# Optimization experiments

Hardware: AMD Instinct MI355X
Metric: run time of the kernel (lower is better)

The kernel has to match this reference:

```python
import jax, jax.numpy as jnp
import numpy as np

E, H, VS, VT, B, S, T = 256, 512, 32000, 32000, 64, 40, 40

def setup_inputs() -> dict:
    key = jax.random.key(0)
    ks = jax.random.split(key, 32)
    def n(k, shape, scale=0.05):
        return (jax.random.normal(k, shape, jnp.float32) * scale)
    return {
        "source_padded": jax.random.randint(ks[0], (B, S), 0, VS),
        "target_padded": jax.random.randint(ks[1], (B, T), 0, VT),
        "source_lengths": jax.random.randint(ks[2], (B,), 2, S + 1),
        "src_emb": n(ks[3], (VS, E)), "tgt_emb": n(ks[4], (VT, E)),
        "Wih_f": n(ks[5], (4 * H, E)), "Whh_f": n(ks[6], (4 * H, H)), "b_f": jnp.zeros((4 * H,), jnp.float32),
        "Wih_b": n(ks[7], (4 * H, E)), "Whh_b": n(ks[8], (4 * H, H)), "b_b": jnp.zeros((4 * H,), jnp.float32),
        "Wih_d": n(ks[9], (4 * H, H + E)), "Whh_d": n(ks[10], (4 * H, H)), "b_d": jnp.zeros((4 * H,), jnp.float32),
        "Whp": n(ks[11], (H, 2 * H)), "bhp": jnp.zeros((H,), jnp.float32),
        "Wcp": n(ks[12], (H, 2 * H)), "bcp": jnp.zeros((H,), jnp.float32),
        "Watt": n(ks[13], (H, 2 * H)), "batt": jnp.zeros((H,), jnp.float32),
        "Wcomb": n(ks[14], (H, 3 * H)), "bcomb": jnp.zeros((H,), jnp.float32),
        "Wvoc": n(ks[15], (VT, H)), "bvoc": jnp.zeros((VT,), jnp.float32),
    }

def _lstm_cell(x, h, c, Wih, Whh, b):
    g = x @ Wih.T + h @ Whh.T + b
    i, f, gg, o = jnp.split(g, 4, axis=-1)  # PyTorch gate order i,f,g,o
    c = jax.nn.sigmoid(f) * c + jax.nn.sigmoid(i) * jnp.tanh(gg)
    h = jax.nn.sigmoid(o) * jnp.tanh(c)
    return h, c

def _masked_scan(X, lengths, Wih, Whh, b):
    # X: [B,S,E]; emulates packed LSTM: state frozen and output zeroed past length
    Bn, Sn, _ = X.shape
    Hn = Whh.shape[1]
    def step(carry, inp):
        h, c = carry
        xt, t = inp
        hn, cn = _lstm_cell(xt, h, c, Wih, Whh, b)
        valid = (t < lengths)[:, None]
        h = jnp.where(valid, hn, h)
        c = jnp.where(valid, cn, c)
        return (h, c), jnp.where(valid, h, 0.0)
    init = (jnp.zeros((Bn, Hn), X.dtype), jnp.zeros((Bn, Hn), X.dtype))
    (h, c), outs = jax.lax.scan(step, init, (X.transpose(1, 0, 2), jnp.arange(Sn)))
    return outs.transpose(1, 0, 2), h, c

def _rev_in_len(X, lengths):
    # reverse each sequence within its own length, zeros elsewhere
    Sn = X.shape[1]
    idx = lengths[:, None] - 1 - jnp.arange(Sn)[None, :]
    g = jnp.take_along_axis(X, jnp.clip(idx, 0)[..., None], axis=1)
    return jnp.where((idx >= 0)[..., None], g, 0.0)

def _forward(source_padded, target_padded, source_lengths,
             src_emb, tgt_emb, Wih_f, Whh_f, b_f, Wih_b, Whh_b, b_b,
             Wih_d, Whh_d, b_d, Whp, bhp, Wcp, bcp, Watt, batt,
             Wcomb, bcomb, Wvoc, bvoc):
    X = src_emb[source_padded]                              # [B,S,E]
    out_f, hf, cf = _masked_scan(X, source_lengths, Wih_f, Whh_f, b_f)
    Xr = _rev_in_len(X, source_lengths)
    out_r, hb, cb = _masked_scan(Xr, source_lengths, Wih_b, Whh_b, b_b)
    out_b = _rev_in_len(out_r, source_lengths)
    enc_hidden = jnp.concatenate([out_f, out_b], axis=-1)   # [B,S,2H]
    dec_h = jnp.concatenate([hf, hb], axis=-1) @ Whp.T + bhp
    dec_c = jnp.concatenate([cf, cb], axis=-1) @ Wcp.T + bcp

    # generate_sent_masks: 1 at positions 1..len-1 (faithful to source), then masked_fill(-inf) where 1
    pos = jnp.arange(S)[None, :]
    enc_masks = (pos >= 1) & (pos < source_lengths[:, None])  # [B,S] bool

    enc_proj = enc_hidden @ Watt.T + batt                    # [B,S,H]
    Y = tgt_emb[target_padded]                               # [B,T,E]
    Hn = Whh_d.shape[1]
    o0 = jnp.zeros((B, Hn), jnp.float32)

    def dec_step(carry, y_t):
        h, c, o_prev = carry
        ybar = jnp.concatenate([y_t, o_prev], axis=-1)
        h, c = _lstm_cell(ybar, h, c, Wih_d, Whh_d, b_d)
        e = jnp.einsum('bsh,bh->bs', enc_proj, h)
        e = jnp.where(enc_masks, -jnp.inf, e)
        alpha = jax.nn.softmax(e, axis=-1)
        a = jnp.einsum('bs,bsd->bd', alpha, enc_hidden)      # [B,2H]
        U = jnp.concatenate([h, a], axis=-1)                 # [B,3H]
        O = jnp.tanh(U @ Wcomb.T + bcomb)                    # dropout eval-mode identity
        return (h, c, O), O

    _, outs = jax.lax.scan(dec_step, (dec_h, dec_c, o0), Y.transpose(1, 0, 2))  # [T,B,H]
    logits = outs @ Wvoc.T + bvoc                            # [T,B,VT]
    logp = jax.nn.log_softmax(logits, axis=-1)
    # CrossEntropyLoss(P.permute(1,2,0), target): mean NLL over all B*T positions
    tgt = target_padded.T[..., None]                         # [T,B,1]
    nll = -jnp.take_along_axis(logp, tgt, axis=-1).squeeze(-1)
    return nll.mean()

def reference(source_padded, target_padded, source_lengths,
              src_emb, tgt_emb, Wih_f, Whh_f, b_f, Wih_b, Whh_b, b_b,
              Wih_d, Whh_d, b_d, Whp, bhp, Wcp, bcp, Watt, batt,
              Wcomb, bcomb, Wvoc, bvoc):
    return _forward(source_padded, target_padded, source_lengths,
                    src_emb, tgt_emb, Wih_f, Whh_f, b_f, Wih_b, Whh_b, b_b,
                    Wih_d, Whh_d, b_d, Whp, bhp, Wcp, bcp, Watt, batt,
                    Wcomb, bcomb, Wvoc, bvoc)
```

## Files before the change

### kernel.cpp

```cpp
#include <hip/hip_runtime.h>
#include <math.h>

#define En 256
#define Hn 512
#define Bn 64
#define Sn 40
#define Tn 40
#define VTn 32000
#define Rn (Tn*Bn)
#define NCH 500

typedef short v8s __attribute__((ext_vector_type(8)));
typedef float v4f __attribute__((ext_vector_type(4)));
typedef _Float16 h2v __attribute__((ext_vector_type(2)));

#if defined(__has_builtin)
#  if __has_builtin(__builtin_amdgcn_fdot2)
#    define HAVE_FDOT2 1
#  endif
#endif

__device__ __forceinline__ float dot4(float4 a, float4 b){
  return a.x*b.x + a.y*b.y + a.z*b.z + a.w*b.w;
}
__device__ __forceinline__ float sigm(float x){ return 1.f/(1.f+__expf(-x)); }
__device__ __forceinline__ unsigned short f2bf(float f){
  unsigned u = __float_as_uint(f);
  unsigned r = u + 0x7FFFu + ((u>>16)&1u);
  return (unsigned short)(r>>16);
}
__device__ __forceinline__ float bf2f(unsigned short u){
  return __uint_as_float(((unsigned)u)<<16);
}
__device__ __forceinline__ unsigned pkbf(float a, float b){
  return (unsigned)f2bf(a) | ((unsigned)f2bf(b)<<16);
}
__device__ __forceinline__ unsigned pkh(float a, float b){
  _Float16 ha = (_Float16)a, hb = (_Float16)b;
  unsigned short ua = __builtin_bit_cast(unsigned short, ha);
  unsigned short ub = __builtin_bit_cast(unsigned short, hb);
  return (unsigned)ua | ((unsigned)ub<<16);
}
__device__ __forceinline__ float fd2(unsigned w, unsigned h, float c){
#ifdef HAVE_FDOT2
  return __builtin_amdgcn_fdot2(__builtin_bit_cast(h2v,w), __builtin_bit_cast(h2v,h), c, false);
#else
  h2v a = __builtin_bit_cast(h2v,w), b = __builtin_bit_cast(h2v,h);
  return c + (float)a[0]*(float)b[0] + (float)a[1]*(float)b[1];
#endif
}

__global__ void prep(float* zero_base,
                     const int* __restrict__ src, const int* __restrict__ tgt,
                     const int* __restrict__ lens, int* __restrict__ grev,
                     int* __restrict__ gtgt,
                     const float* __restrict__ Whh_f, unsigned short* __restrict__ Whf16,
                     const float* __restrict__ Whh_b, unsigned short* __restrict__ Whb16,
                     const float* __restrict__ Whh_d, const float* __restrict__ Wih_d,
                     unsigned short* __restrict__ Wd16,
                     const float* __restrict__ Wcomb, unsigned short* __restrict__ Wc16){
  int blk = blockIdx.x, tid = threadIdx.x;
  if (blk < 224){
    ((float4*)zero_base)[blk*256 + tid] = make_float4(0.f,0.f,0.f,0.f);
    return;
  }
  blk -= 224;
  if (blk < 10){
    int r = blk*256 + tid;
    if (r < Bn*Sn){
      int b = r/Sn, s = r%Sn;
      int j = lens[b]-1-s;
      grev[r] = (j>=0) ? src[b*Sn+j] : -1;
      int t2 = r>>6, b2 = r&63;
      gtgt[r] = tgt[b2*Tn + t2];
    }
    return;
  }
  blk -= 10;
  if (blk < 512){
    size_t e = ((size_t)blk*256 + tid)*8;
    float4 a = *(const float4*)(Whh_f+e), b = *(const float4*)(Whh_f+e+4);
    uint4 u; u.x=pkbf(a.x,a.y); u.y=pkbf(a.z,a.w); u.z=pkbf(b.x,b.y); u.w=pkbf(b.z,b.w);
    *(uint4*)(Whf16+e) = u;
    return;
  }
  blk -= 512;
  if (blk < 512){
    size_t e = ((size_t)blk*256 + tid)*8;
    float4 a = *(const float4*)(Whh_b+e), b = *(const float4*)(Whh_b+e+4);
    uint4 u; u.x=pkbf(a.x,a.y); u.y=pkbf(a.z,a.w); u.z=pkbf(b.x,b.y); u.w=pkbf(b.z,b.w);
    *(uint4*)(Whb16+e) = u;
    return;
  }
  blk -= 512;
  if (blk < 1024){
    size_t e = ((size_t)blk*256 + tid)*8;
    int row = (int)(e>>10), k = (int)(e&1023);
    const float* sp = (k<512) ? (Whh_d + (size_t)row*512 + k)
                              : (Wih_d + (size_t)row*768 + 256 + (k-512));
    float4 a = *(const float4*)sp, b = *(const float4*)(sp+4);
    uint4 u; u.x=pkbf(a.x,a.y); u.y=pkbf(a.z,a.w); u.z=pkbf(b.x,b.y); u.w=pkbf(b.z,b.w);
    *(uint4*)(Wd16+e) = u;
    return;
  }
  blk -= 1024;
  {
    size_t e = ((size_t)blk*256 + tid)*8;
    float4 a = *(const float4*)(Wcomb+e), b = *(const float4*)(Wcomb+e+4);
    uint4 u; u.x=pkh(a.x,a.y); u.y=pkh(a.z,a.w); u.z=pkh(b.x,b.y); u.w=pkh(b.z,b.w);
    *(uint4*)(Wc16+e) = u;
  }
}

struct GArg {
  const float* A; const int* gth; int lda;
  const float* B; int ldb;
  const float* bias; float* C; int ldc; int K;
};
struct GArg3 { GArg a[3]; };

__global__ __launch_bounds__(256) void ggemm(GArg3 p3){
  GArg d = p3.a[blockIdx.z];
  __shared__ unsigned short Abf[128*64];
  __shared__ unsigned short Bbf[128*64];
  const int n0 = blockIdx.x*128, r0 = blockIdx.y*128;
  const int tid = threadIdx.x;
  const int w = tid>>6, lane = tid&63;
  const int wr = w>>1, wc = w&1;
  v4f acc[4][4];
#pragma unroll
  for (int i=0;i<4;++i)
#pragma unroll
    for (int j=0;j<4;++j) acc[i][j] = (v4f){0.f,0.f,0.f,0.f};
  const int srow = tid>>1, kc = (tid&1)*32;
  int ar = d.gth ? d.gth[r0+srow] : (r0+srow);
  const float* Arow = (ar>=0) ? (d.A + (size_t)ar*d.lda) : nullptr;
  const float* Brow = d.B + (size_t)(n0+srow)*d.ldb;
  for (int kb=0; kb<d.K; kb+=64){
    __syncthreads();
#pragma unroll
    for (int c=0;c<4;++c){
      int k = kc + c*8;
      int swz = k ^ ((srow&7)<<3);
      uint4 ua;
      if (Arow){
        float4 x0 = *(const float4*)(Arow+kb+k);
        float4 x1 = *(const float4*)(Arow+kb+k+4);
        ua.x=pkbf(x0.x,x0.y); ua.y=pkbf(x0.z,x0.w); ua.z=pkbf(x1.x,x1.y); ua.w=pkbf(x1.z,x1.w);
      } else ua = make_uint4(0,0,0,0);
      *(uint4*)&Abf[srow*64 + swz] = ua;
      float4 y0 = *(const float4*)(Brow+kb+k);
      float4 y1 = *(const float4*)(Brow+kb+k+4);
      uint4 ub; ub.x=pkbf(y0.x,y0.y); ub.y=pkbf(y0.z,y0.w); ub.z=pkbf(y1.x,y1.y); ub.w=pkbf(y1.z,y1.w);
      *(uint4*)&Bbf[srow*64 + swz] = ub;
    }
    __syncthreads();
#pragma unroll
    for (int kk=0; kk<64; kk+=32){
      int kfr = kk + (lane>>4)*8;
      v8s bfr[4];
#pragma unroll
      for (int ni=0;ni<4;++ni){
        int brow = wc*64 + ni*16 + (lane&15);
        bfr[ni] = *(const v8s*)&Bbf[brow*64 + (kfr ^ ((brow&7)<<3))];
      }
#pragma unroll
      for (int mi=0;mi<4;++mi){
        int arl = wr*64 + mi*16 + (lane&15);
        v8s af = *(const v8s*)&Abf[arl*64 + (kfr ^ ((arl&7)<<3))];
#pragma unroll
        for (int ni=0;ni<4;++ni)
          acc[mi][ni] = __builtin_amdgcn_mfma_f32_16x16x32_bf16(af, bfr[ni], acc[mi][ni], 0,0,0);
      }
    }
  }
#pragma unroll
  for (int ni=0;ni<4;++ni){
    int col = n0 + wc*64 + ni*16 + (lane&15);
    float bb = d.bias[col];
#pragma unroll
    for (int mi=0;mi<4;++mi)
#pragma unroll
      for (int r=0;r<4;++r){
        int row = r0 + wr*64 + mi*16 + (lane>>4)*4 + r;
        d.C[(size_t)row*d.ldc + col] = acc[mi][ni][r] + bb;
      }
  }
}

__global__ __launch_bounds__(256) void enc_step(
    const unsigned short* __restrict__ hf_in, unsigned short* __restrict__ hf_out,
    const unsigned short* __restrict__ hb_in, unsigned short* __restrict__ hb_out,
    float* __restrict__ cF, float* __restrict__ cB,
    const unsigned short* __restrict__ Wf16, const unsigned short* __restrict__ Wb16,
    const float* __restrict__ Gf, const float* __restrict__ Gb,
    float* __restrict__ encH, float* __restrict__ outR,
    const int* __restrict__ lens, int s){
  __shared__ unsigned short Wls[64*64];
  __shared__ unsigned short Hls[64*64];
  __shared__ float Cls[64][66];
  const int bx = blockIdx.x;
  const int dir = bx>>5;
  const int u0 = (bx&31)*16;
  const unsigned short* W16 = dir ? Wb16 : Wf16;
  const unsigned short* hin = dir ? hb_in : hf_in;
  unsigned short* hout      = dir ? hb_out : hf_out;
  float* c = dir ? cB : cF;
  const float* G = dir ? Gb : Gf;
  const int tid = threadIdx.x, w = tid>>6, lane = tid&63;
  v4f acc[4];
#pragma unroll
  for (int ni=0;ni<4;++ni) acc[ni] = (v4f){0.f,0.f,0.f,0.f};
  const int l = tid>>2;
  const int kc4 = (tid&3)*16;
  const int grow = (l>>4)*512 + u0 + (l&15);
  const unsigned short* Wrow = W16 + (size_t)grow*512;
  const unsigned short* Hrow = hin + (size_t)l*512;
  for (int kb=0; kb<512; kb+=64){
    __syncthreads();
#pragma unroll
    for (int c2=0;c2<2;++c2){
      int k = kc4 + c2*8;
      int swz = k ^ ((l&7)<<3);
      *(uint4*)&Wls[l*64+swz] = *(const uint4*)(Wrow + kb + k);
      *(uint4*)&Hls[l*64+swz] = *(const uint4*)(Hrow + kb + k);
    }
    __syncthreads();
#pragma unroll
    for (int kk=0; kk<64; kk+=32){
      int kfr = kk + (lane>>4)*8;
      int mrow = w*16 + (lane&15);
      v8s af = *(const v8s*)&Wls[mrow*64 + (kfr ^ ((mrow&7)<<3))];
#pragma unroll
      for (int ni=0;ni<4;++ni){
        int brow = ni*16 + (lane&15);
        v8s bf = *(const v8s*)&Hls[brow*64 + (kfr ^ ((brow&7)<<3))];
        acc[ni] = __builtin_amdgcn_mfma_f32_16x16x32_bf16(af, bf, acc[ni], 0,0,0);
      }
    }
  }
#pragma unroll
  for (int ni=0;ni<4;++ni)
#pragma unroll
    for (int r=0;r<4;++r)
      Cls[w*16 + (lane>>4)*4 + r][ni*16 + (lane&15)] = acc[ni][r];
  __syncthreads();
  const int u_l = tid&15, bq = tid>>4;
#pragma unroll
  for (int j=0;j<4;++j){
    int b = bq + j*16;
    size_t gidx = ((size_t)(b*Sn+s))*2048 + u0 + u_l;
    float gi = Cls[u_l][b]      + G[gidx];
    float gf = Cls[16+u_l][b]   + G[gidx+512];
    float gg = Cls[32+u_l][b]   + G[gidx+1024];
    float go = Cls[48+u_l][b]   + G[gidx+1536];
    int bu = b*512 + u0 + u_l;
    bool valid = s < lens[b];
    float cp = c[bu];
    float cn = sigm(gf)*cp + sigm(gi)*tanhf(gg);
    float hn = sigm(go)*tanhf(cn);
    c[bu] = valid ? cn : cp;
    hout[bu] = valid ? f2bf(hn) : hin[bu];
    if (dir==0) encH[((size_t)(b*Sn+s))*1024 + u0+u_l] = valid ? hn : 0.f;
    else        outR[((size_t)(b*Sn+s))*512  + u0+u_l] = valid ? hn : 0.f;
  }
}

__global__ void mid_fused(const unsigned short* __restrict__ h16f,
                          const unsigned short* __restrict__ h16b,
                          const float* __restrict__ cF, const float* __restrict__ cB,
                          const float* __restrict__ Whp, const float* __restrict__ bhp,
                          const float* __restrict__ Wcp, const float* __restrict__ bcp,
                          unsigned short* __restrict__ ho0, float* __restrict__ dC,
                          const float* __restrict__ outR, const int* __restrict__ lens,
                          float* __restrict__ encH,
                          const float* __restrict__ Wvoc, unsigned short* __restrict__ W16){
  int blk = blockIdx.x, tid = threadIdx.x;
  if (blk < 128){
    int isC = blk >= 64;
    int idx = (blk & 63)*256 + tid;
#pragma unroll
    for (int e=0;e<2;++e){
      int o = idx*2 + e;
      int b = o>>9, u = o&511;
      if (!isC){
        const float* wr = Whp + (size_t)u*1024;
        float acc = bhp[u];
        const uint4* hf4 = (const uint4*)(h16f + (size_t)b*512);
        for (int q=0;q<64;++q){
          uint4 v = hf4[q];
          unsigned uu[4] = {v.x,v.y,v.z,v.w};
#pragma unroll
          for (int i2=0;i2<4;++i2){
            acc += bf2f((unsigned short)(uu[i2]&0xFFFF))*wr[q*8+i2*2];
            acc += bf2f((unsigned short)(uu[i2]>>16))   *wr[q*8+i2*2+1];
          }
        }
        const uint4* hb4 = (const uint4*)(h16b + (size_t)b*512);
        const float* wr2 = wr + 512;
        for (int q=0;q<64;++q){
          uint4 v = hb4[q];
          unsigned uu[4] = {v.x,v.y,v.z,v.w};
#pragma unroll
          for (int i2=0;i2<4;++i2){
            acc += bf2f((unsigned short)(uu[i2]&0xFFFF))*wr2[q*8+i2*2];
            acc += bf2f((unsigned short)(uu[i2]>>16))   *wr2[q*8+i2*2+1];
          }
        }
        ho0[b*1024 + u] = f2bf(acc);
      } else {
        const float4* w4 = (const float4*)(Wcp + (size_t)u*1024);
        float acc = bcp[u];
        const float4* x1 = (const float4*)(cF + (size_t)b*512);
        const float4* x2 = (const float4*)(cB + (size_t)b*512);
        for (int q=0;q<128;++q) acc += dot4(x1[q], w4[q]);
        for (int q=0;q<128;++q) acc += dot4(x2[q], w4[128+q]);
        dC[b*512 + u] = acc;
      }
    }
    return;
  }
  blk -= 128;
  if (blk < 640){
    int e = (blk*256 + tid)*8;
    int u = e & 511;
    int bsi = e >> 9;
    int s = bsi % Sn, b = bsi / Sn;
    int len = lens[b];
    float4 v0 = make_float4(0,0,0,0), v1 = make_float4(0,0,0,0);
    if (s < len){
      int j = len-1-s;
      const float* sp = outR + ((size_t)(b*Sn+j))*512 + u;
      v0 = *(const float4*)sp; v1 = *(const float4*)(sp+4);
    }
    float* dp = encH + ((size_t)(b*Sn+s))*1024 + 512 + u;
    *(float4*)dp = v0; *(float4*)(dp+4) = v1;
    return;
  }
  blk -= 640;
  {
    size_t e = ((size_t)blk*256 + tid)*8;
    float4 a = *(const float4*)(Wvoc+e), b = *(const float4*)(Wvoc+e+4);
    uint4 u; u.x=pkbf(a.x,a.y); u.y=pkbf(a.z,a.w); u.z=pkbf(b.x,b.y); u.w=pkbf(b.z,b.w);
    *(uint4*)(W16+e) = u;
  }
}

__global__ __launch_bounds__(256) void dec_gates(
    const unsigned short* __restrict__ Wd16, const unsigned short* __restrict__ ho_cur,
    unsigned short* __restrict__ ho_next, const float* __restrict__ Gdy,
    float* __restrict__ dC, int t){
  __shared__ unsigned short Wls[64*64];
  __shared__ unsigned short Hls[64*64];
  __shared__ float Cls[64][66];
  const int u0 = blockIdx.x*16;
  const int tid = threadIdx.x, w = tid>>6, lane = tid&63;
  v4f acc[4];
#pragma unroll
  for (int ni=0;ni<4;++ni) acc[ni] = (v4f){0.f,0.f,0.f,0.f};
  const int l = tid>>2;
  const int kc4 = (tid&3)*16;
  const int grow = (l>>4)*512 + u0 + (l&15);
  const unsigned short* Wrow = Wd16 + (size_t)grow*1024;
  const unsigned short* Hrow = ho_cur + (size_t)l*1024;
  for (int kb=0; kb<1024; kb+=64){
    __syncthreads();
#pragma unroll
    for (int c2=0;c2<2;++c2){
      int k = kc4 + c2*8;
      int swz = k ^ ((l&7)<<3);
      *(uint4*)&Wls[l*64+swz] = *(const uint4*)(Wrow + kb + k);
      *(uint4*)&Hls[l*64+swz] = *(const uint4*)(Hrow + kb + k);
    }
    __syncthreads();
#pragma unroll
    for (int kk=0; kk<64; kk+=32){
      int kfr = kk + (lane>>4)*8;
      int mrow = w*16 + (lane&15);
      v8s af = *(const v8s*)&Wls[mrow*64 + (kfr ^ ((mrow&7)<<3))];
#pragma unroll
      for (int ni=0;ni<4;++ni){
        int brow = ni*16 + (lane&15);
        v8s bf = *(const v8s*)&Hls[brow*64 + (kfr ^ ((brow&7)<<3))];
        acc[ni] = __builtin_amdgcn_mfma_f32_16x16x32_bf16(af, bf, acc[ni], 0,0,0);
      }
    }
  }
#pragma unroll
  for (int ni=0;ni<4;++ni)
#pragma unroll
    for (int r=0;r<4;++r)
      Cls[w*16 + (lane>>4)*4 + r][ni*16 + (lane&15)] = acc[ni][r];
  __syncthreads();
  const int u_l = tid&15, bq = tid>>4;
#pragma unroll
  for (int j=0;j<4;++j){
    int b = bq + j*16;
    size_t gidx = ((size_t)(t*Bn+b))*2048 + u0 + u_l;
    float gi = Cls[u_l][b]      + Gdy[gidx];
    float gf = Cls[16+u_l][b]   + Gdy[gidx+512];
    float gg = Cls[32+u_l][b]   + Gdy[gidx+1024];
    float go = Cls[48+u_l][b]   + Gdy[gidx+1536];
    int bu = b*512 + u0 + u_l;
    float cp = dC[bu];
    float cn = sigm(gf)*cp + sigm(gi)*tanhf(gg);
    float hn = sigm(go)*tanhf(cn);
    dC[bu] = cn;
    ho_next[b*1024 + u0 + u_l] = f2bf(hn);
  }
}

__global__ __launch_bounds__(256) void dec_attcomb(
    unsigned short* __restrict__ ho_next, const float* __restrict__ eprj,
    const float* __restrict__ encH, const int* __restrict__ lens,
    const unsigned short* __restrict__ Wc16, const float* __restrict__ bcomb,
    unsigned short* __restrict__ A16, int t){
  const int b = blockIdx.x >> 2;
  const int q = blockIdx.x & 3;
  const int tid = threadIdx.x;
  __shared__ __align__(16) float hs[512];
  __shared__ __align__(16) float als[1024];
  __shared__ float es[Sn], sal[Sn];
  __shared__ float sinv;
  __shared__ __align__(16) unsigned int ha16[768];
  __shared__ float ps[128][2];
  for (int i=tid; i<512; i+=256) hs[i] = bf2f(ho_next[b*1024 + i]);
  __syncthreads();
  const int wv = tid>>6, lane = tid&63;
  const int len = lens[b];
  for (int si=0; si<10; ++si){
    int s2 = wv*10 + si;
    const float* pr = eprj + ((size_t)(b*Sn+s2))*512 + lane*8;
    float4 p0 = *(const float4*)pr, p1 = *(const float4*)(pr+4);
    const float* hh = hs + lane*8;
    float4 h0 = *(const float4*)hh, h1 = *(const float4*)(hh+4);
    float a = dot4(p0,h0) + dot4(p1,h1);
#pragma unroll
    for (int off=32; off; off>>=1) a += __shfl_down(a, off);
    if (lane==0) es[s2] = (s2>=1 && s2<len) ? -INFINITY : a;
  }
  __syncthreads();
  if (tid < 64){
    float e2 = (tid<Sn) ? es[tid] : -INFINITY;
    float m = e2;
#pragma unroll
    for (int off=32; off; off>>=1) m = fmaxf(m, __shfl_xor(m, off));
    float p = (tid<Sn) ? __expf(e2-m) : 0.f;
    float sum = p;
#pragma unroll
    for (int off=32; off; off>>=1) sum += __shfl_xor(sum, off);
    if (tid<Sn) sal[tid] = p;
    if (tid==0) sinv = 1.f/sum;
  }
  __syncthreads();
  float inv = sinv;
#pragma unroll
  for (int dq=0; dq<4; ++dq){
    int d = dq*256 + tid;
    float acc = 0.f;
    for (int s2=0; s2<Sn; ++s2) acc += sal[s2]*encH[((size_t)(b*Sn+s2))*1024 + d];
    als[d] = acc*inv;
  }
  __syncthreads();
  for (int p=tid; p<768; p+=256){
    int i0 = 2*p, i1 = 2*p+1;
    float x0 = (i0<512) ? hs[i0] : als[i0-512];
    float x1 = (i1<512) ? hs[i1] : als[i1-512];
    ha16[p] = pkh(x0, x1);
  }
  __syncthreads();
  const int rloc = tid & 127;
  const int kh = tid >> 7;
  const int row = q*128 + rloc;
  const uint4* wp = (const uint4*)(Wc16 + (size_t)row*1536 + kh*768);
  const uint4* hp = (const uint4*)&ha16[kh*384];
  float a0 = 0.f;
#pragma unroll 4
  for (int qq=0; qq<96; ++qq){
    uint4 wv4 = wp[qq];
    uint4 hv4 = hp[qq];
    a0 = fd2(wv4.x, hv4.x, a0);
    a0 = fd2(wv4.y, hv4.y, a0);
    a0 = fd2(wv4.z, hv4.z, a0);
    a0 = fd2(wv4.w, hv4.w, a0);
  }
  ps[rloc][kh] = a0;
  __syncthreads();
  if (tid < 128){
    int r2 = q*128 + tid;
    float O = tanhf(ps[tid][0] + ps[tid][1] + bcomb[r2]);
    unsigned short ob = f2bf(O);
    ho_next[b*1024 + 512 + r2] = ob;
    A16[((size_t)(t*Bn+b))*512 + r2] = ob;
  }
}

__global__ __launch_bounds__(256,1) void vocab_mfma(
    const unsigned short* __restrict__ A16, const unsigned short* __restrict__ W16,
    const float* __restrict__ bv, float* __restrict__ stats){
  __shared__ unsigned short Abf[256*64];
  __shared__ unsigned short Bbf[128*64];
  const int vb = blockIdx.x, rb = blockIdx.y;
  const int r0 = rb*256, v0 = vb*128;
  const int tid = threadIdx.x, w = tid>>6, lane = tid&63;
  const int wr = w>>1, wc = w&1;
  v4f acc[8][4];
#pragma unroll
  for (int i=0;i<8;++i)
#pragma unroll
    for (int j=0;j<4;++j) acc[i][j] = (v4f){0.f,0.f,0.f,0.f};
  const unsigned short* Arow = A16 + (size_t)(r0+tid)*512;
  const int srow2 = tid>>1, kc2 = (tid&1)*32;
  const unsigned short* Brow = W16 + (size_t)(v0+srow2)*512;
  for (int kb=0; kb<512; kb+=64){
    __syncthreads();
#pragma unroll
    for (int c=0;c<8;++c){
      int k = c*8;
      *(uint4*)&Abf[tid*64 + (k ^ ((tid&7)<<3))] = *(const uint4*)(Arow + kb + k);
    }
#pragma unroll
    for (int c=0;c<4;++c){
      int k = kc2 + c*8;
      *(uint4*)&Bbf[srow2*64 + (k ^ ((srow2&7)<<3))] = *(const uint4*)(Brow + kb + k);
    }
    __syncthreads();
#pragma unroll
    for (int kk=0; kk<64; kk+=32){
      int kfr = kk + (lane>>4)*8;
      v8s bfr[4];
#pragma unroll
      for (int ni=0;ni<4;++ni){
        int brow = wc*64 + ni*16 + (lane&15);
        bfr[ni] = *(const v8s*)&Bbf[brow*64 + (kfr ^ ((brow&7)<<3))];
      }
#pragma unroll
      for (int mi=0;mi<8;++mi){
        int arow = wr*128 + mi*16 + (lane&15);
        v8s af = *(const v8s*)&Abf[arow*64 + (kfr ^ ((arow&7)<<3))];
#pragma unroll
        for (int ni=0;ni<4;++ni)
          acc[mi][ni] = __builtin_amdgcn_mfma_f32_16x16x32_bf16(af, bfr[ni], acc[mi][ni], 0,0,0);
      }
    }
  }
  float bj[4];
#pragma unroll
  for (int ni=0;ni<4;++ni) bj[ni] = bv[v0 + wc*64 + ni*16 + (lane&15)];
#pragma unroll
  for (int mi=0;mi<8;++mi){
#pragma unroll
    for (int r=0;r<4;++r){
      float x0 = acc[mi][0][r]+bj[0], x1 = acc[mi][1][r]+bj[1];
      float x2 = acc[mi][2][r]+bj[2], x3 = acc[mi][3][r]+bj[3];
      float mx = fmaxf(fmaxf(x0,x1), fmaxf(x2,x3));
#pragma unroll
      for (int off=1; off<16; off<<=1) mx = fmaxf(mx, __shfl_xor(mx, off));
      float se = __expf(x0-mx)+__expf(x1-mx)+__expf(x2-mx)+__expf(x3-mx);
#pragma unroll
      for (int off=1; off<16; off<<=1) se += __shfl_xor(se, off);
      if ((lane&15)==0){
        int row = r0 + wr*128 + mi*16 + (lane>>4)*4 + r;
        int chunk = vb*2 + wc;
        size_t o = ((size_t)row*NCH + chunk)*2;
        stats[o] = mx; stats[o+1] = se;
      }
    }
  }
}

__global__ void tail(const float* __restrict__ stats, const unsigned short* __restrict__ A16,
                     const float* __restrict__ Wvoc, const float* __restrict__ bvoc,
                     const int* __restrict__ gtgt, float* __restrict__ out){
  int r = blockIdx.x*4 + (threadIdx.x>>6);
  int lane = threadIdx.x & 63;
  const float* st = stats + (size_t)r*NCH*2;
  float M = -INFINITY;
  for (int c=lane; c<NCH; c+=64) M = fmaxf(M, st[2*c]);
#pragma unroll
  for (int off=32; off; off>>=1) M = fmaxf(M, __shfl_xor(M, off));
  float S = 0.f;
  for (int c=lane; c<NCH; c+=64) S += __expf(st[2*c]-M)*st[2*c+1];
#pragma unroll
  for (int off=32; off; off>>=1) S += __shfl_xor(S, off);
  int v = gtgt[r];
  int k = lane*8;
  uint4 a4 = *(const uint4*)(A16 + (size_t)r*512 + k);
  const float* wvp = Wvoc + (size_t)v*512 + k;
  float4 w0 = *(const float4*)wvp, w1 = *(const float4*)(wvp+4);
  unsigned uu[4] = {a4.x, a4.y, a4.z, a4.w};
  float dot = 0.f;
  dot += bf2f((unsigned short)(uu[0]&0xFFFF))*w0.x + bf2f((unsigned short)(uu[0]>>16))*w0.y;
  dot += bf2f((unsigned short)(uu[1]&0xFFFF))*w0.z + bf2f((unsigned short)(uu[1]>>16))*w0.w;
  dot += bf2f((unsigned short)(uu[2]&0xFFFF))*w1.x + bf2f((unsigned short)(uu[2]>>16))*w1.y;
  dot += bf2f((unsigned short)(uu[3]&0xFFFF))*w1.z + bf2f((unsigned short)(uu[3]>>16))*w1.w;
#pragma unroll
  for (int off=32; off; off>>=1) dot += __shfl_down(dot, off);
  if (lane==0){
    float lse = M + logf(S);
    float nll = lse - (dot + bvoc[v]);
    atomicAdd(out, nll * (1.0f/(float)Rn));
  }
}

extern "C" void kernel_launch(void* const* d_in, const int* in_sizes, int n_in,
                              void* d_out, int out_size, void* d_ws, size_t ws_size,
                              hipStream_t stream){
  (void)in_sizes; (void)n_in; (void)out_size; (void)ws_size;
  const int*   srcP  = (const int*)  d_in[0];
  const int*   tgtP  = (const int*)  d_in[1];
  const int*   lens  = (const int*)  d_in[2];
  const float* semb  = (const float*)d_in[3];
  const float* temb  = (const float*)d_in[4];
  const float* Wih_f = (const float*)d_in[5];
  const float* Whh_f = (const float*)d_in[6];
  const float* b_f   = (const float*)d_in[7];
  const float* Wih_b = (const float*)d_in[8];
  const float* Whh_b = (const float*)d_in[9];
  const float* b_b   = (const float*)d_in[10];
  const float* Wih_d = (const float*)d_in[11];
  const float* Whh_d = (const float*)d_in[12];
  const float* b_d   = (const float*)d_in[13];
  const float* Whp   = (const float*)d_in[14];
  const float* bhp   = (const float*)d_in[15];
  const float* Wcp   = (const float*)d_in[16];
  const float* bcp   = (const float*)d_in[17];
  const float* Watt  = (const float*)d_in[18];
  const float* batt  = (const float*)d_in[19];
  const float* Wcomb = (const float*)d_in[20];
  const float* bcomb = (const float*)d_in[21];
  const float* Wvoc  = (const float*)d_in[22];
  const float* bvoc  = (const float*)d_in[23];

  float* w = (float*)d_ws;
  size_t off = 0;
  auto alloc = [&](size_t n){ float* p = w + off; off += n; return p; };
  float* encH = alloc(2621440);
  float* outR = alloc(1310720);
  float* eprj = alloc(1310720);
  float* Gf   = alloc(5242880);
  float* Gb   = alloc(5242880);
  float* Gdy  = alloc(5242880);
  unsigned short* A16   = (unsigned short*)alloc(655360);
  unsigned short* Whf16 = (unsigned short*)alloc(524288);
  unsigned short* Whb16 = (unsigned short*)alloc(524288);
  unsigned short* Wd16  = (unsigned short*)alloc(1048576);
  unsigned short* Wc16  = (unsigned short*)alloc(393216);
  float* zero_base = w + off;
  float* cF = alloc(32768);
  float* cB = alloc(32768);
  float* dC = alloc(32768);
  unsigned short* h16f[2] = {(unsigned short*)alloc(16384), (unsigned short*)alloc(16384)};
  unsigned short* h16b[2] = {(unsigned short*)alloc(16384), (unsigned short*)alloc(16384)};
  unsigned short* ho[2]   = {(unsigned short*)alloc(32768), (unsigned short*)alloc(32768)};
  int* grev = (int*)alloc(2560);
  int* gtgt = (int*)alloc(2560);
  unsigned short* W16 = (unsigned short*)Gf;
  float* stats = encH;

  hipMemsetAsync(d_out, 0, sizeof(float), stream);
  prep<<<2666, 256, 0, stream>>>(zero_base, srcP, tgtP, lens, grev, gtgt,
                                 Whh_f, Whf16, Whh_b, Whb16, Whh_d, Wih_d, Wd16,
                                 Wcomb, Wc16);
  {
    GArg3 g;
    g.a[0] = GArg{semb, srcP, En, Wih_f, En,  b_f, Gf,  2048, En};
    g.a[1] = GArg{semb, grev, En, Wih_b, En,  b_b, Gb,  2048, En};
    g.a[2] = GArg{temb, gtgt, En, Wih_d, 768, b_d, Gdy, 2048, En};
    ggemm<<<dim3(16,20,3), 256, 0, stream>>>(g);
  }
  for (int s=0; s<Sn; ++s)
    enc_step<<<64, 256, 0, stream>>>(h16f[s&1], h16f[(s+1)&1], h16b[s&1], h16b[(s+1)&1],
                                     cF, cB, Whf16, Whb16, Gf, Gb, encH, outR, lens, s);
  mid_fused<<<8768, 256, 0, stream>>>(h16f[0], h16b[0], cF, cB, Whp, bhp, Wcp, bcp,
                                      ho[0], dC, outR, lens, encH, Wvoc, W16);
  {
    GArg3 g;
    g.a[0] = GArg{encH, nullptr, 1024, Watt, 1024, batt, eprj, 512, 1024};
    g.a[1] = g.a[0]; g.a[2] = g.a[0];
    ggemm<<<dim3(4,20,1), 256, 0, stream>>>(g);
  }
  for (int t=0; t<Tn; ++t){
    dec_gates<<<32, 256, 0, stream>>>(Wd16, ho[t&1], ho[(t+1)&1], Gdy, dC, t);
    dec_attcomb<<<256, 256, 0, stream>>>(ho[(t+1)&1], eprj, encH, lens, Wc16, bcomb, A16, t);
  }
  vocab_mfma<<<dim3(VTn/128, Rn/256), 256, 0, stream>>>(A16, W16, bvoc, stats);
  tail<<<Rn/4, 256, 0, stream>>>(stats, A16, Wvoc, bvoc, gtgt, (float*)d_out);
}
```

Baseline: 2.440 ms.

## Persist encoder scan with grid barrier, merge decoder steps, retile vocab GEMM

Replaces the 40 per-step encoder launches with one persistent 64-block kernel that synchronises steps through an atomic spin barrier. The decoder's gates and attention/combine kernels become one launch per step: 64 blocks compute attention output for step t-1 and 32 blocks compute gates for step t, which spin on a counter before reading the new output. The vocab GEMM drops from 256-row to 128-row tiles with a different staging layout. The intent is to cut launch overhead and overlap decoder phases; the risks are deadlock if blocks are not co-resident, spin cost, and fewer MFMA per loaded tile.

```diff
diff --git a/kernel.cpp b/kernel.cpp
--- a/kernel.cpp
+++ b/kernel.cpp
@@ -60,11 +60,11 @@
                      unsigned short* __restrict__ Wd16,
                      const float* __restrict__ Wcomb, unsigned short* __restrict__ Wc16){
   int blk = blockIdx.x, tid = threadIdx.x;
-  if (blk < 224){
+  if (blk < 209){
     ((float4*)zero_base)[blk*256 + tid] = make_float4(0.f,0.f,0.f,0.f);
     return;
   }
-  blk -= 224;
+  blk -= 209;
   if (blk < 10){
     int r = blk*256 + tid;
     if (r < Bn*Sn){
@@ -188,14 +188,14 @@
   }
 }
 
-__global__ __launch_bounds__(256) void enc_step(
-    const unsigned short* __restrict__ hf_in, unsigned short* __restrict__ hf_out,
-    const unsigned short* __restrict__ hb_in, unsigned short* __restrict__ hb_out,
+__global__ __launch_bounds__(256) void enc_scan(
+    unsigned short* __restrict__ hf0, unsigned short* __restrict__ hf1,
+    unsigned short* __restrict__ hb0, unsigned short* __restrict__ hb1,
     float* __restrict__ cF, float* __restrict__ cB,
     const unsigned short* __restrict__ Wf16, const unsigned short* __restrict__ Wb16,
     const float* __restrict__ Gf, const float* __restrict__ Gb,
     float* __restrict__ encH, float* __restrict__ outR,
-    const int* __restrict__ lens, int s){
+    const int* __restrict__ lens, int* __restrict__ bar){
   __shared__ unsigned short Wls[64*64];
   __shared__ unsigned short Hls[64*64];
   __shared__ float Cls[64][66];
@@ -203,66 +203,82 @@
   const int dir = bx>>5;
   const int u0 = (bx&31)*16;
   const unsigned short* W16 = dir ? Wb16 : Wf16;
-  const unsigned short* hin = dir ? hb_in : hf_in;
-  unsigned short* hout      = dir ? hb_out : hf_out;
   float* c = dir ? cB : cF;
   const float* G = dir ? Gb : Gf;
   const int tid = threadIdx.x, w = tid>>6, lane = tid&63;
-  v4f acc[4];
-#pragma unroll
-  for (int ni=0;ni<4;++ni) acc[ni] = (v4f){0.f,0.f,0.f,0.f};
   const int l = tid>>2;
   const int kc4 = (tid&3)*16;
   const int grow = (l>>4)*512 + u0 + (l&15);
   const unsigned short* Wrow = W16 + (size_t)grow*512;
-  const unsigned short* Hrow = hin + (size_t)l*512;
-  for (int kb=0; kb<512; kb+=64){
-    __syncthreads();
-#pragma unroll
-    for (int c2=0;c2<2;++c2){
-      int k = kc4 + c2*8;
-      int swz = k ^ ((l&7)<<3);
-      *(uint4*)&Wls[l*64+swz] = *(const uint4*)(Wrow + kb + k);
-      *(uint4*)&Hls[l*64+swz] = *(const uint4*)(Hrow + kb + k);
-    }
-    __syncthreads();
-#pragma unroll
-    for (int kk=0; kk<64; kk+=32){
-      int kfr = kk + (lane>>4)*8;
-      int mrow = w*16 + (lane&15);
-      v8s af = *(const v8s*)&Wls[mrow*64 + (kfr ^ ((mrow&7)<<3))];
-#pragma unroll
-      for (int ni=0;ni<4;++ni){
-        int brow = ni*16 + (lane&15);
-        v8s bf = *(const v8s*)&Hls[brow*64 + (kfr ^ ((brow&7)<<3))];
-        acc[ni] = __builtin_amdgcn_mfma_f32_16x16x32_bf16(af, bf, acc[ni], 0,0,0);
-      }
-    }
-  }
-#pragma unroll
-  for (int ni=0;ni<4;++ni)
-#pragma unroll
-    for (int r=0;r<4;++r)
-      Cls[w*16 + (lane>>4)*4 + r][ni*16 + (lane&15)] = acc[ni][r];
-  __syncthreads();
-  const int u_l = tid&15, bq = tid>>4;
-#pragma unroll
-  for (int j=0;j<4;++j){
-    int b = bq + j*16;
-    size_t gidx = ((size_t)(b*Sn+s))*2048 + u0 + u_l;
-    float gi = Cls[u_l][b]      + G[gidx];
-    float gf = Cls[16+u_l][b]   + G[gidx+512];
-    float gg = Cls[32+u_l][b]   + G[gidx+1024];
-    float go = Cls[48+u_l][b]   + G[gidx+1536];
-    int bu = b*512 + u0 + u_l;
-    bool valid = s < lens[b];
-    float cp = c[bu];
-    float cn = sigm(gf)*cp + sigm(gi)*tanhf(gg);
-    float hn = sigm(go)*tanhf(cn);
-    c[bu] = valid ? cn : cp;
-    hout[bu] = valid ? f2bf(hn) : hin[bu];
-    if (dir==0) encH[((size_t)(b*Sn+s))*1024 + u0+u_l] = valid ? hn : 0.f;
-    else        outR[((size_t)(b*Sn+s))*512  + u0+u_l] = valid ? hn : 0.f;
+#pragma unroll 1
+  for (int s=0; s<Sn; ++s){
+    const unsigned short* hin = dir ? ((s&1)?hb1:hb0) : ((s&1)?hf1:hf0);
+    unsigned short* hout      = dir ? ((s&1)?hb0:hb1) : ((s&1)?hf0:hf1);
+    const unsigned short* Hrow = hin + (size_t)l*512;
+    v4f acc[4];
+#pragma unroll
+    for (int ni=0;ni<4;++ni) acc[ni] = (v4f){0.f,0.f,0.f,0.f};
+    for (int kb=0; kb<512; kb+=64){
+      __syncthreads();
+#pragma unroll
+      for (int c2=0;c2<2;++c2){
+        int k = kc4 + c2*8;
+        int swz = k ^ ((l&7)<<3);
+        *(uint4*)&Wls[l*64+swz] = *(const uint4*)(Wrow + kb + k);
+        *(uint4*)&Hls[l*64+swz] = *(const uint4*)(Hrow + kb + k);
+      }
+      __syncthreads();
+#pragma unroll
+      for (int kk=0; kk<64; kk+=32){
+        int kfr = kk + (lane>>4)*8;
+        int mrow = w*16 + (lane&15);
+        v8s af = *(const v8s*)&Wls[mrow*64 + (kfr ^ ((mrow&7)<<3))];
+#pragma unroll
+        for (int ni=0;ni<4;++ni){
+          int brow = ni*16 + (lane&15);
+          v8s bf = *(const v8s*)&Hls[brow*64 + (kfr ^ ((brow&7)<<3))];
+          acc[ni] = __builtin_amdgcn_mfma_f32_16x16x32_bf16(af, bf, acc[ni], 0,0,0);
+        }
+      }
+    }
+#pragma unroll
+    for (int ni=0;ni<4;++ni)
+#pragma unroll
+      for (int r=0;r<4;++r)
+        Cls[w*16 + (lane>>4)*4 + r][ni*16 + (lane&15)] = acc[ni][r];
+    __syncthreads();
+    const int u_l = tid&15, bq = tid>>4;
+#pragma unroll
+    for (int j=0;j<4;++j){
+      int b = bq + j*16;
+      size_t gidx = ((size_t)(b*Sn+s))*2048 + u0 + u_l;
+      float gi = Cls[u_l][b]      + G[gidx];
+      float gf = Cls[16+u_l][b]   + G[gidx+512];
+      float gg = Cls[32+u_l][b]   + G[gidx+1024];
+      float go = Cls[48+u_l][b]   + G[gidx+1536];
+      int bu = b*512 + u0 + u_l;
+      bool valid = s < lens[b];
+      float cp = c[bu];
+      float cn = sigm(gf)*cp + sigm(gi)*tanhf(gg);
+      float hn = sigm(go)*tanhf(cn);
+      c[bu] = valid ? cn : cp;
+      hout[bu] = valid ? f2bf(hn) : hin[bu];
+      if (dir==0) encH[((size_t)(b*Sn+s))*1024 + u0+u_l] = valid ? hn : 0.f;
+      else        outR[((size_t)(b*Sn+s))*512  + u0+u_l] = valid ? hn : 0.f;
+    }
+    if (s < Sn-1){
+      __syncthreads();
+      if (tid==0){
+        __threadfence();
+        __hip_atomic_fetch_add(bar, 1, __ATOMIC_RELEASE, __HIP_MEMORY_SCOPE_AGENT);
+        const int target = 64*(s+1);
+        long it = 0;
+        while (__hip_atomic_load(bar, __ATOMIC_ACQUIRE, __HIP_MEMORY_SCOPE_AGENT) < target
+               && it < 2000000000L) ++it;
+      }
+      __syncthreads();
+      __threadfence();
+    }
   }
 }
 
@@ -271,7 +287,7 @@
                           const float* __restrict__ cF, const float* __restrict__ cB,
                           const float* __restrict__ Whp, const float* __restrict__ bhp,
                           const float* __restrict__ Wcp, const float* __restrict__ bcp,
-                          unsigned short* __restrict__ ho0, float* __restrict__ dC,
+                          unsigned short* __restrict__ H0, float* __restrict__ dC,
                           const float* __restrict__ outR, const int* __restrict__ lens,
                           float* __restrict__ encH,
                           const float* __restrict__ Wvoc, unsigned short* __restrict__ W16){
@@ -307,7 +323,7 @@
             acc += bf2f((unsigned short)(uu[i2]>>16))   *wr2[q*8+i2*2+1];
           }
         }
-        ho0[b*1024 + u] = f2bf(acc);
+        H0[b*512 + u] = f2bf(acc);
       } else {
         const float4* w4 = (const float4*)(Wcp + (size_t)u*1024);
         float acc = bcp[u];
@@ -346,15 +362,101 @@
   }
 }
 
-__global__ __launch_bounds__(256) void dec_gates(
-    const unsigned short* __restrict__ Wd16, const unsigned short* __restrict__ ho_cur,
-    unsigned short* __restrict__ ho_next, const float* __restrict__ Gdy,
-    float* __restrict__ dC, int t){
+__global__ __launch_bounds__(256) void dec_step(
+    const unsigned short* __restrict__ Wd16,
+    const unsigned short* __restrict__ Hcur, unsigned short* __restrict__ Hnext,
+    unsigned short* __restrict__ obuf,
+    const float* __restrict__ Gdy, float* __restrict__ dC,
+    const float* __restrict__ eprj, const float* __restrict__ encH,
+    const int* __restrict__ lens,
+    const unsigned short* __restrict__ Wc16, const float* __restrict__ bcomb,
+    unsigned short* __restrict__ A16, int* __restrict__ cnt, int t){
+  const int blk = blockIdx.x, tid = threadIdx.x;
+  if (blk < Bn){
+    if (t == 0) return;
+    const int b = blk;
+    __shared__ __align__(16) float hs[512];
+    __shared__ __align__(16) float als[1024];
+    __shared__ float es[Sn], sal[Sn];
+    __shared__ float sinv;
+    __shared__ __align__(16) unsigned ha16[768];
+    for (int i=tid; i<512; i+=256) hs[i] = bf2f(Hcur[b*512 + i]);
+    __syncthreads();
+    const int wv = tid>>6, lane = tid&63;
+    const int len = lens[b];
+    for (int si=0; si<10; ++si){
+      int s2 = wv*10 + si;
+      const float* pr = eprj + ((size_t)(b*Sn+s2))*512 + lane*8;
+      float4 p0 = *(const float4*)pr, p1 = *(const float4*)(pr+4);
+      const float* hh = hs + lane*8;
+      float4 h0 = *(const float4*)hh, h1 = *(const float4*)(hh+4);
+      float a = dot4(p0,h0) + dot4(p1,h1);
+#pragma unroll
+      for (int off=32; off; off>>=1) a += __shfl_down(a, off);
+      if (lane==0) es[s2] = (s2>=1 && s2<len) ? -INFINITY : a;
+    }
+    __syncthreads();
+    if (tid < 64){
+      float e2 = (tid<Sn) ? es[tid] : -INFINITY;
+      float m = e2;
+#pragma unroll
+      for (int off=32; off; off>>=1) m = fmaxf(m, __shfl_xor(m, off));
+      float p = (tid<Sn) ? __expf(e2-m) : 0.f;
+      float sum = p;
+#pragma unroll
+      for (int off=32; off; off>>=1) sum += __shfl_xor(sum, off);
+      if (tid<Sn) sal[tid] = p;
+      if (tid==0) sinv = 1.f/sum;
+    }
+    __syncthreads();
+    float inv = sinv;
+#pragma unroll
+    for (int dq=0; dq<4; ++dq){
+      int d = dq*256 + tid;
+      float acc = 0.f;
+      for (int s2=0; s2<Sn; ++s2) acc += sal[s2]*encH[((size_t)(b*Sn+s2))*1024 + d];
+      als[d] = acc*inv;
+    }
+    __syncthreads();
+    for (int p=tid; p<768; p+=256){
+      int i0 = 2*p, i1 = 2*p+1;
+      float x0 = (i0<512) ? hs[i0] : als[i0-512];
+      float x1 = (i1<512) ? hs[i1] : als[i1-512];
+      ha16[p] = pkh(x0, x1);
+    }
+    __syncthreads();
+    const uint4* hp = (const uint4*)ha16;
+#pragma unroll
+    for (int rr=0; rr<2; ++rr){
+      int row = tid + rr*256;
+      const uint4* wp = (const uint4*)(Wc16 + (size_t)row*1536);
+      float a0 = 0.f;
+#pragma unroll 4
+      for (int qq=0; qq<192; ++qq){
+        uint4 w4 = wp[qq];
+        uint4 h4 = hp[qq];
+        a0 = fd2(w4.x, h4.x, a0);
+        a0 = fd2(w4.y, h4.y, a0);
+        a0 = fd2(w4.z, h4.z, a0);
+        a0 = fd2(w4.w, h4.w, a0);
+      }
+      float O = tanhf(a0 + bcomb[row]);
+      unsigned short ob = f2bf(O);
+      obuf[b*512 + row] = ob;
+      A16[((size_t)((t-1)*Bn + b))*512 + row] = ob;
+    }
+    __threadfence();
+    __syncthreads();
+    if (tid==0)
+      __hip_atomic_fetch_add(&cnt[t], 1, __ATOMIC_RELEASE, __HIP_MEMORY_SCOPE_AGENT);
+    return;
+  }
+  if (t == Tn) return;
   __shared__ unsigned short Wls[64*64];
   __shared__ unsigned short Hls[64*64];
   __shared__ float Cls[64][66];
-  const int u0 = blockIdx.x*16;
-  const int tid = threadIdx.x, w = tid>>6, lane = tid&63;
+  const int u0 = (blk - Bn)*16;
+  const int w = tid>>6, lane = tid&63;
   v4f acc[4];
 #pragma unroll
   for (int ni=0;ni<4;++ni) acc[ni] = (v4f){0.f,0.f,0.f,0.f};
@@ -362,15 +464,27 @@
   const int kc4 = (tid&3)*16;
   const int grow = (l>>4)*512 + u0 + (l&15);
   const unsigned short* Wrow = Wd16 + (size_t)grow*1024;
-  const unsigned short* Hrow = ho_cur + (size_t)l*1024;
-  for (int kb=0; kb<1024; kb+=64){
+  const int kmax = t ? 1024 : 512;
+  for (int kb=0; kb<kmax; kb+=64){
+    if (kb == 512){
+      __syncthreads();
+      if (tid==0){
+        long it = 0;
+        while (__hip_atomic_load(&cnt[t], __ATOMIC_ACQUIRE, __HIP_MEMORY_SCOPE_AGENT) < Bn
+               && it < 2000000000L) ++it;
+      }
+      __syncthreads();
+      __threadfence();
+    }
+    const unsigned short* src = (kb < 512) ? (Hcur + (size_t)l*512 + kb)
+                                           : (obuf + (size_t)l*512 + (kb-512));
     __syncthreads();
 #pragma unroll
     for (int c2=0;c2<2;++c2){
       int k = kc4 + c2*8;
       int swz = k ^ ((l&7)<<3);
       *(uint4*)&Wls[l*64+swz] = *(const uint4*)(Wrow + kb + k);
-      *(uint4*)&Hls[l*64+swz] = *(const uint4*)(Hrow + kb + k);
+      *(uint4*)&Hls[l*64+swz] = *(const uint4*)(src + k);
     }
     __syncthreads();
 #pragma unroll
@@ -406,149 +520,68 @@
     float cn = sigm(gf)*cp + sigm(gi)*tanhf(gg);
     float hn = sigm(go)*tanhf(cn);
     dC[bu] = cn;
-    ho_next[b*1024 + u0 + u_l] = f2bf(hn);
-  }
-}
-
-__global__ __launch_bounds__(256) void dec_attcomb(
-    unsigned short* __restrict__ ho_next, const float* __restrict__ eprj,
-    const float* __restrict__ encH, const int* __restrict__ lens,
-    const unsigned short* __restrict__ Wc16, const float* __restrict__ bcomb,
-    unsigned short* __restrict__ A16, int t){
-  const int b = blockIdx.x >> 2;
-  const int q = blockIdx.x & 3;
-  const int tid = threadIdx.x;
-  __shared__ __align__(16) float hs[512];
-  __shared__ __align__(16) float als[1024];
-  __shared__ float es[Sn], sal[Sn];
-  __shared__ float sinv;
-  __shared__ __align__(16) unsigned int ha16[768];
-  __shared__ float ps[128][2];
-  for (int i=tid; i<512; i+=256) hs[i] = bf2f(ho_next[b*1024 + i]);
-  __syncthreads();
-  const int wv = tid>>6, lane = tid&63;
-  const int len = lens[b];
-  for (int si=0; si<10; ++si){
-    int s2 = wv*10 + si;
-    const float* pr = eprj + ((size_t)(b*Sn+s2))*512 + lane*8;
-    float4 p0 = *(const float4*)pr, p1 = *(const float4*)(pr+4);
-    const float* hh = hs + lane*8;
-    float4 h0 = *(const float4*)hh, h1 = *(const float4*)(hh+4);
-    float a = dot4(p0,h0) + dot4(p1,h1);
-#pragma unroll
-    for (int off=32; off; off>>=1) a += __shfl_down(a, off);
-    if (lane==0) es[s2] = (s2>=1 && s2<len) ? -INFINITY : a;
-  }
-  __syncthreads();
-  if (tid < 64){
-    float e2 = (tid<Sn) ? es[tid] : -INFINITY;
-    float m = e2;
-#pragma unroll
-    for (int off=32; off; off>>=1) m = fmaxf(m, __shfl_xor(m, off));
-    float p = (tid<Sn) ? __expf(e2-m) : 0.f;
-    float sum = p;
-#pragma unroll
-    for (int off=32; off; off>>=1) sum += __shfl_xor(sum, off);
-    if (tid<Sn) sal[tid] = p;
-    if (tid==0) sinv = 1.f/sum;
-  }
-  __syncthreads();
-  float inv = sinv;
-#pragma unroll
-  for (int dq=0; dq<4; ++dq){
-    int d = dq*256 + tid;
-    float acc = 0.f;
-    for (int s2=0; s2<Sn; ++s2) acc += sal[s2]*encH[((size_t)(b*Sn+s2))*1024 + d];
-    als[d] = acc*inv;
-  }
-  __syncthreads();
-  for (int p=tid; p<768; p+=256){
-    int i0 = 2*p, i1 = 2*p+1;
-    float x0 = (i0<512) ? hs[i0] : als[i0-512];
-    float x1 = (i1<512) ? hs[i1] : als[i1-512];
-    ha16[p] = pkh(x0, x1);
-  }
-  __syncthreads();
-  const int rloc = tid & 127;
-  const int kh = tid >> 7;
-  const int row = q*128 + rloc;
-  const uint4* wp = (const uint4*)(Wc16 + (size_t)row*1536 + kh*768);
-  const uint4* hp = (const uint4*)&ha16[kh*384];
-  float a0 = 0.f;
-#pragma unroll 4
-  for (int qq=0; qq<96; ++qq){
-    uint4 wv4 = wp[qq];
-    uint4 hv4 = hp[qq];
-    a0 = fd2(wv4.x, hv4.x, a0);
-    a0 = fd2(wv4.y, hv4.y, a0);
-    a0 = fd2(wv4.z, hv4.z, a0);
-    a0 = fd2(wv4.w, hv4.w, a0);
-  }
-  ps[rloc][kh] = a0;
-  __syncthreads();
-  if (tid < 128){
-    int r2 = q*128 + tid;
-    float O = tanhf(ps[tid][0] + ps[tid][1] + bcomb[r2]);
-    unsigned short ob = f2bf(O);
-    ho_next[b*1024 + 512 + r2] = ob;
-    A16[((size_t)(t*Bn+b))*512 + r2] = ob;
-  }
-}
-
-__global__ __launch_bounds__(256,1) void vocab_mfma(
+    Hnext[b*512 + u0 + u_l] = f2bf(hn);
+  }
+}
+
+__global__ __launch_bounds__(256) void vocab_mfma(
     const unsigned short* __restrict__ A16, const unsigned short* __restrict__ W16,
     const float* __restrict__ bv, float* __restrict__ stats){
-  __shared__ unsigned short Abf[256*64];
+  __shared__ unsigned short Abf[128*64];
   __shared__ unsigned short Bbf[128*64];
   const int vb = blockIdx.x, rb = blockIdx.y;
-  const int r0 = rb*256, v0 = vb*128;
-  const int tid = threadIdx.x, w = tid>>6, lane = tid&63;
+  const int r0 = rb*128, v0 = vb*128;
+  const int tid = threadIdx.x;
+  const int w = tid>>6, lane = tid&63;
   const int wr = w>>1, wc = w&1;
-  v4f acc[8][4];
-#pragma unroll
-  for (int i=0;i<8;++i)
+  v4f acc[4][4];
+#pragma unroll
+  for (int i=0;i<4;++i)
 #pragma unroll
     for (int j=0;j<4;++j) acc[i][j] = (v4f){0.f,0.f,0.f,0.f};
-  const unsigned short* Arow = A16 + (size_t)(r0+tid)*512;
-  const int srow2 = tid>>1, kc2 = (tid&1)*32;
-  const unsigned short* Brow = W16 + (size_t)(v0+srow2)*512;
-  for (int kb=0; kb<512; kb+=64){
-    __syncthreads();
-#pragma unroll
-    for (int c=0;c<8;++c){
-      int k = c*8;
-      *(uint4*)&Abf[tid*64 + (k ^ ((tid&7)<<3))] = *(const uint4*)(Arow + kb + k);
-    }
+  const int srow = tid>>1;
+  const int sk0  = (tid&1)*8;
+  const int arow = wr*64 + (lane&15);
+  const int brow = wc*64 + (lane&15);
+  const int kfrag = (lane>>4)*8;
+  for (int ks=0; ks<8; ++ks){
+    const int kb = ks*64;
+    __syncthreads();
 #pragma unroll
     for (int c=0;c<4;++c){
-      int k = kc2 + c*8;
-      *(uint4*)&Bbf[srow2*64 + (k ^ ((srow2&7)<<3))] = *(const uint4*)(Brow + kb + k);
+      int k = sk0 + c*16;
+      int swz = k ^ ((srow&7)<<3);
+      *(uint4*)&Abf[srow*64 + swz] = *(const uint4*)(A16 + (size_t)(r0+srow)*512 + kb + k);
+      *(uint4*)&Bbf[srow*64 + swz] = *(const uint4*)(W16 + (size_t)(v0+srow)*512 + kb + k);
     }
     __syncthreads();
 #pragma unroll
     for (int kk=0; kk<64; kk+=32){
-      int kfr = kk + (lane>>4)*8;
-      v8s bfr[4];
+      v8s af[4], bf[4];
+#pragma unroll
+      for (int mi=0;mi<4;++mi){
+        int row = arow + mi*16;
+        int k = kk + kfrag;
+        af[mi] = *(const v8s*)&Abf[row*64 + (k ^ ((row&7)<<3))];
+      }
 #pragma unroll
       for (int ni=0;ni<4;++ni){
-        int brow = wc*64 + ni*16 + (lane&15);
-        bfr[ni] = *(const v8s*)&Bbf[brow*64 + (kfr ^ ((brow&7)<<3))];
-      }
-#pragma unroll
-      for (int mi=0;mi<8;++mi){
-        int arow = wr*128 + mi*16 + (lane&15);
-        v8s af = *(const v8s*)&Abf[arow*64 + (kfr ^ ((arow&7)<<3))];
+        int row = brow + ni*16;
+        int k = kk + kfrag;
+        bf[ni] = *(const v8s*)&Bbf[row*64 + (k ^ ((row&7)<<3))];
+      }
+#pragma unroll
+      for (int mi=0;mi<4;++mi)
 #pragma unroll
         for (int ni=0;ni<4;++ni)
-          acc[mi][ni] = __builtin_amdgcn_mfma_f32_16x16x32_bf16(af, bfr[ni], acc[mi][ni], 0,0,0);
-      }
+          acc[mi][ni] = __builtin_amdgcn_mfma_f32_16x16x32_bf16(af[mi], bf[ni], acc[mi][ni], 0,0,0);
     }
   }
   float bj[4];
 #pragma unroll
   for (int ni=0;ni<4;++ni) bj[ni] = bv[v0 + wc*64 + ni*16 + (lane&15)];
 #pragma unroll
-  for (int mi=0;mi<8;++mi){
+  for (int mi=0;mi<4;++mi){
 #pragma unroll
     for (int r=0;r<4;++r){
       float x0 = acc[mi][0][r]+bj[0], x1 = acc[mi][1][r]+bj[1];
@@ -560,10 +593,11 @@
 #pragma unroll
       for (int off=1; off<16; off<<=1) se += __shfl_xor(se, off);
       if ((lane&15)==0){
-        int row = r0 + wr*128 + mi*16 + (lane>>4)*4 + r;
+        int row = r0 + wr*64 + mi*16 + (lane>>4)*4 + r;
         int chunk = vb*2 + wc;
         size_t o = ((size_t)row*NCH + chunk)*2;
-        stats[o] = mx; stats[o+1] = se;
+        stats[o]   = mx;
+        stats[o+1] = se;
       }
     }
   }
@@ -650,16 +684,21 @@
   float* cF = alloc(32768);
   float* cB = alloc(32768);
   float* dC = alloc(32768);
-  unsigned short* h16f[2] = {(unsigned short*)alloc(16384), (unsigned short*)alloc(16384)};
-  unsigned short* h16b[2] = {(unsigned short*)alloc(16384), (unsigned short*)alloc(16384)};
-  unsigned short* ho[2]   = {(unsigned short*)alloc(32768), (unsigned short*)alloc(32768)};
+  unsigned short* h16f0 = (unsigned short*)alloc(16384);
+  unsigned short* h16f1 = (unsigned short*)alloc(16384);
+  unsigned short* h16b0 = (unsigned short*)alloc(16384);
+  unsigned short* h16b1 = (unsigned short*)alloc(16384);
+  unsigned short* H0    = (unsigned short*)alloc(16384);
+  unsigned short* H1    = (unsigned short*)alloc(16384);
+  unsigned short* obuf  = (unsigned short*)alloc(16384);
+  int* syncv = (int*)alloc(1024);
   int* grev = (int*)alloc(2560);
   int* gtgt = (int*)alloc(2560);
   unsigned short* W16 = (unsigned short*)Gf;
   float* stats = encH;
 
   hipMemsetAsync(d_out, 0, sizeof(float), stream);
-  prep<<<2666, 256, 0, stream>>>(zero_base, srcP, tgtP, lens, grev, gtgt,
+  prep<<<2651, 256, 0, stream>>>(zero_base, srcP, tgtP, lens, grev, gtgt,
                                  Whh_f, Whf16, Whh_b, Whb16, Whh_d, Wih_d, Wd16,
                                  Wcomb, Wc16);
   {
@@ -669,21 +708,20 @@
     g.a[2] = GArg{temb, gtgt, En, Wih_d, 768, b_d, Gdy, 2048, En};
     ggemm<<<dim3(16,20,3), 256, 0, stream>>>(g);
   }
-  for (int s=0; s<Sn; ++s)
-    enc_step<<<64, 256, 0, stream>>>(h16f[s&1], h16f[(s+1)&1], h16b[s&1], h16b[(s+1)&1],
-                                     cF, cB, Whf16, Whb16, Gf, Gb, encH, outR, lens, s);
-  mid_fused<<<8768, 256, 0, stream>>>(h16f[0], h16b[0], cF, cB, Whp, bhp, Wcp, bcp,
-                                      ho[0], dC, outR, lens, encH, Wvoc, W16);
+  enc_scan<<<64, 256, 0, stream>>>(h16f0, h16f1, h16b0, h16b1, cF, cB,
+                                   Whf16, Whb16, Gf, Gb, encH, outR, lens, syncv);
+  mid_fused<<<8768, 256, 0, stream>>>(h16f0, h16b0, cF, cB, Whp, bhp, Wcp, bcp,
+                                      H0, dC, outR, lens, encH, Wvoc, W16);
   {
     GArg3 g;
     g.a[0] = GArg{encH, nullptr, 1024, Watt, 1024, batt, eprj, 512, 1024};
     g.a[1] = g.a[0]; g.a[2] = g.a[0];
     ggemm<<<dim3(4,20,1), 256, 0, stream>>>(g);
   }
-  for (int t=0; t<Tn; ++t){
-    dec_gates<<<32, 256, 0, stream>>>(Wd16, ho[t&1], ho[(t+1)&1], Gdy, dC, t);
-    dec_attcomb<<<256, 256, 0, stream>>>(ho[(t+1)&1], eprj, encH, lens, Wc16, bcomb, A16, t);
-  }
-  vocab_mfma<<<dim3(VTn/128, Rn/256), 256, 0, stream>>>(A16, W16, bvoc, stats);
+  unsigned short* Hb[2] = {H0, H1};
+  for (int t=0; t<=Tn; ++t)
+    dec_step<<<96, 256, 0, stream>>>(Wd16, Hb[t&1], Hb[(t+1)&1], obuf, Gdy, dC,
+                                     eprj, encH, lens, Wc16, bcomb, A16, syncv, t);
+  vocab_mfma<<<dim3(VTn/128, Rn/128), 256, 0, stream>>>(A16, W16, bvoc, stats);
   tail<<<Rn/4, 256, 0, stream>>>(stats, A16, Wvoc, bvoc, gtgt, (float*)d_out);
 }
```

Result: slower. 4.412 ms (+80.8%).
